# Performance work log

Hardware: AMD Instinct MI355X
Metric: run time of the kernel (lower is better)

Reference implementation:

```python
import math
import jax, jax.numpy as jnp
import numpy as np

HIDDEN = 2048
NUM_HEADS = 32
HEAD_DIM = HIDDEN // NUM_HEADS
NUM_BLOCKS = 4
INTER = 2 * HIDDEN
EPS = 1e-5
ROPE_THETA = 10000.0


def setup_inputs() -> dict:
    key = jax.random.key(0)
    ks = jax.random.split(key, 6)
    B, S = 2, 2048
    sc = 0.02
    return {
        "x": jax.random.normal(ks[0], (B, S, HIDDEN), jnp.float32),
        "attn_norm_w": jnp.ones((HIDDEN,), jnp.float32),
        "ffn_norm_w": jnp.ones((HIDDEN,), jnp.float32),
        "w_qkv": jax.random.normal(ks[1], (3 * HIDDEN, HIDDEN), jnp.float32) * sc,
        "w_o": jax.random.normal(ks[2], (HIDDEN, HIDDEN), jnp.float32) * sc,
        "w_up": jax.random.normal(ks[3], (2 * INTER, HIDDEN), jnp.float32) * sc,
        "w_down": jax.random.normal(ks[4], (HIDDEN, INTER), jnp.float32) * sc,
    }


def _rmsnorm(x, w):
    var = jnp.mean(x * x, axis=-1, keepdims=True)
    return x * jax.lax.rsqrt(var + EPS) * w


def _rope_cache(seq_len, dim, theta, scale):
    inv_freq = 1.0 / (theta ** (jnp.arange(0, dim, 2, dtype=jnp.float32) / dim))
    t = jnp.arange(seq_len, dtype=jnp.float32) / scale
    freqs = jnp.outer(t, inv_freq)                     # [S, D/2]
    emb = jnp.concatenate([freqs, freqs], axis=-1)     # [S, D]
    return jnp.cos(emb), jnp.sin(emb)


def _apply_rope(x, cos, sin):
    # x: [B, H, S, D]
    d2 = x.shape[-1] // 2
    x1, x2 = x[..., :d2], x[..., d2:]
    rot = jnp.concatenate([-x2, x1], axis=-1)
    return x * cos[None, None] + rot * sin[None, None]


def reference(x, attn_norm_w, ffn_norm_w, w_qkv, w_o, w_up, w_down):
    B, S, _ = x.shape
    residual = x
    h = _rmsnorm(x, attn_norm_w)

    qkv = jnp.einsum('bsh,oh->bso', h, w_qkv)
    qkv = qkv.reshape(B, S, 3, NUM_HEADS, HEAD_DIM)
    q, k, v = qkv[:, :, 0], qkv[:, :, 1], qkv[:, :, 2]
    q = q.transpose(0, 2, 1, 3)  # [B,H,S,D]
    k = k.transpose(0, 2, 1, 3)
    v = v.transpose(0, 2, 1, 3)

    cos, sin = _rope_cache(S, HEAD_DIM, ROPE_THETA, 1.0)
    q = _apply_rope(q, cos, sin)
    k = _apply_rope(k, cos, sin)

    scale = 1.0 / math.sqrt(HEAD_DIM)
    attn = jnp.einsum('bhqd,bhkd->bhqk', q, k) * scale

    num_blocks = max(1, min(NUM_BLOCKS, S))
    blk = math.ceil(S / num_blocks)
    pos = jnp.arange(S)
    block_ids = pos // blk
    block_mask = block_ids[:, None] != block_ids[None, :]
    causal_mask = pos[:, None] < pos[None, :]
    invalid = causal_mask | block_mask                 # [S,S]
    mask_floor = jnp.finfo(attn.dtype).min
    attn = jnp.where(invalid[None, None], mask_floor, attn)

    attn = jax.nn.softmax(attn, axis=-1)
    context = jnp.einsum('bhqk,bhkd->bhqd', attn, v)
    context = context.transpose(0, 2, 1, 3).reshape(B, S, HIDDEN)

    x = residual + jnp.einsum('bsh,oh->bso', context, w_o)

    residual = x
    h = _rmsnorm(x, ffn_norm_w)
    up = jnp.einsum('bsh,oh->bso', h, w_up)
    gate, value = up[..., :INTER], up[..., INTER:]
    down = jnp.einsum('bsi,oi->bso', jax.nn.silu(gate) * value, w_down)
    return residual + down
```

## Files before the change

kernel.cpp:

```cpp
#include <hip/hip_runtime.h>
#include <cstdint>
#include <cstddef>

typedef __bf16 bf16x8 __attribute__((ext_vector_type(8)));
typedef __bf16 bf16x4 __attribute__((ext_vector_type(4)));
typedef float  f32x4  __attribute__((ext_vector_type(4)));

#define TOKENS  4096
#define SEQLEN  2048
#define HID     2048
#define QKV_W   6144
#define UP_W    8192
#define INTER_  4096

__device__ __forceinline__ void async16(const void* g, void* l) {
  __builtin_amdgcn_global_load_lds(
      (__attribute__((address_space(1))) void*)(g),
      (__attribute__((address_space(3))) void*)(l), 16, 0, 0);
}

__global__ __launch_bounds__(256) void cvt_kernel(const float* __restrict__ src,
                                                  __bf16* __restrict__ dst, int n4) {
  int i = blockIdx.x * 256 + threadIdx.x;
  if (i >= n4) return;
  float4 f = ((const float4*)src)[i];
  bf16x4 o;
  o[0] = (__bf16)f.x; o[1] = (__bf16)f.y; o[2] = (__bf16)f.z; o[3] = (__bf16)f.w;
  ((bf16x4*)dst)[i] = o;
}

__global__ __launch_bounds__(256) void rmsnorm_kernel(const float* __restrict__ x,
                                                      const float* __restrict__ wgt,
                                                      __bf16* __restrict__ out) {
  const int tok = blockIdx.x;
  const int t = threadIdx.x;
  const float4* xr = (const float4*)(x + (long)tok * HID);
  float4 a = xr[t], b = xr[t + 256];
  float ss = a.x*a.x + a.y*a.y + a.z*a.z + a.w*a.w
           + b.x*b.x + b.y*b.y + b.z*b.z + b.w*b.w;
  #pragma unroll
  for (int off = 32; off; off >>= 1) ss += __shfl_xor(ss, off);
  __shared__ float red[4];
  if ((t & 63) == 0) red[t >> 6] = ss;
  __syncthreads();
  float tot = red[0] + red[1] + red[2] + red[3];
  float r = rsqrtf(tot * (1.0f / HID) + 1e-5f);
  const float4* wr = (const float4*)wgt;
  float4 wa = wr[t], wb = wr[t + 256];
  bf16x4 o0, o1;
  o0[0] = (__bf16)(a.x * r * wa.x); o0[1] = (__bf16)(a.y * r * wa.y);
  o0[2] = (__bf16)(a.z * r * wa.z); o0[3] = (__bf16)(a.w * r * wa.w);
  o1[0] = (__bf16)(b.x * r * wb.x); o1[1] = (__bf16)(b.y * r * wb.y);
  o1[2] = (__bf16)(b.z * r * wb.z); o1[3] = (__bf16)(b.w * r * wb.w);
  bf16x4* orow = (bf16x4*)(out + (long)tok * HID);
  orow[t] = o0; orow[t + 256] = o1;
}

template<bool OUT_BF16, bool ADD_RES, bool ROPE, bool SILU>
__global__ __launch_bounds__(256) void gemm_bt(const __bf16* __restrict__ A, int lda,
                                               const __bf16* __restrict__ B, int ldb,
                                               void* Cv, int ldc,
                                               const float* __restrict__ Res, int K) {
  __shared__ __align__(16) __bf16 As[128 * 64];
  __shared__ __align__(16) __bf16 Bs[128 * 64];
  const int t = threadIdx.x;
  const int lane = t & 63;
  const int w = t >> 6;
  const int wm = (w >> 1) * 64, wn = (w & 1) * 64;
  const int m0 = blockIdx.y * 128;
  const int n0 = SILU ? blockIdx.x * 64 : blockIdx.x * 128;
  const int sr = t >> 3;
  const int sc = (((t & 7) ^ (sr & 7)) * 8);
  const __bf16* Ag = A + (long)(m0 + sr) * lda + sc;
  const __bf16* Bg = B + (long)(n0 + sr) * ldb + sc;
  char* lA = (char*)As + t * 16;
  char* lB = (char*)Bs + t * 16;
  const int lr = lane & 15;
  const int lq = lane >> 4;
  f32x4 acc[4][4] = {};
  for (int k0 = 0; k0 < K; k0 += 64) {
    __syncthreads();
    #pragma unroll
    for (int c = 0; c < 4; c++)
      async16(Ag + (long)(c * 32) * lda + k0, lA + c * 4096);
    #pragma unroll
    for (int c = 0; c < 4; c++) {
      const long rowoff = SILU ? (long)((c & 1) * INTER_ + (c >> 1) * 32) * ldb
                               : (long)(c * 32) * ldb;
      async16(Bg + rowoff + k0, lB + c * 4096);
    }
    __syncthreads();
    #pragma unroll
    for (int ks = 0; ks < 2; ks++) {
      const int pos = (((ks * 4 + lq) ^ (lr & 7)) * 8);
      bf16x8 af[4], bfr[4];
      #pragma unroll
      for (int i = 0; i < 4; i++)
        af[i]  = *(const bf16x8*)(As + (wm + i * 16 + lr) * 64 + pos);
      #pragma unroll
      for (int j = 0; j < 4; j++)
        bfr[j] = *(const bf16x8*)(Bs + (wn + j * 16 + lr) * 64 + pos);
      #pragma unroll
      for (int i = 0; i < 4; i++)
        #pragma unroll
        for (int j = 0; j < 4; j++)
          acc[i][j] = __builtin_amdgcn_mfma_f32_16x16x32_bf16(af[i], bfr[j], acc[i][j], 0, 0, 0);
    }
  }
  const int lq4 = lq * 4;
  #pragma unroll
  for (int i = 0; i < 4; i++) {
    #pragma unroll
    for (int r = 0; r < 4; r++) {
      const long row = m0 + wm + i * 16 + lq4 + r;
      #pragma unroll
      for (int j = 0; j < 4; j++) {
        const long col = n0 + wn + j * 16 + lr;
        float v = acc[i][j][r];
        if (ADD_RES) v += Res[row * (long)ldc + col];
        if (OUT_BF16) ((__bf16*)Cv)[row * (long)ldc + col] = (__bf16)v;
        else          ((float*)Cv)[row * (long)ldc + col] = v;
      }
    }
  }
}

template<bool ROPE, bool SILU>
__global__ __launch_bounds__(512, 2) void gemm8p(const __bf16* __restrict__ A, int lda,
                                                 const __bf16* __restrict__ B, int ldb,
                                                 void* Cv, int ldc, int K) {
  __shared__ __align__(16) __bf16 As[2 * 16384];
  __shared__ __align__(16) __bf16 Bs[2 * 16384];
  const int tid  = threadIdx.x;
  const int lane = tid & 63;
  const int w    = tid >> 6;
  const int wm2  = w >> 2;
  const int wn4  = w & 3;
  const int lr   = lane & 15;
  const int lq   = lane >> 4;
  const int m0   = blockIdx.y * 256;
  const int n0   = ROPE ? blockIdx.x * 256 : 0;
  const int n0c  = SILU ? blockIdx.x * 128 : 0;

  const long r0 = tid >> 3;
  const int  e  = (((tid & 7) ^ ((int)r0 & 7)) * 8);
  const __bf16* Ap0 = A + (long)(m0 + r0) * lda + e;
  long br0, br1, bhs;
  if (ROPE) {
    br0 = n0 + 64 * (((int)r0 >> 5) & 3) + ((int)r0 & 31);
    br1 = n0 + 64 * ((((int)r0 + 64) >> 5) & 3) + ((int)r0 & 31);
    bhs = 32 * (long)ldb;
  } else {
    br0 = n0c + r0;
    br1 = n0c + r0 + 64;
    bhs = (long)INTER_ * ldb;
  }
  const __bf16* Bp0 = B + br0 * ldb + e;
  const __bf16* Bp1 = B + br1 * ldb + e;
  char* sA = (char*)As;
  char* sB = (char*)Bs;
  const int tid16 = tid * 16;

#define STAGE_A(h_, nb_, kk_) do {                                                     \
    async16(Ap0 + (long)((h_) * 128) * lda + (kk_),      sA + (nb_)*32768 + (h_)*16384 + tid16);        \
    async16(Ap0 + (long)((h_) * 128 + 64) * lda + (kk_), sA + (nb_)*32768 + (h_)*16384 + 8192 + tid16); \
  } while (0)
#define STAGE_B(h_, nb_, kk_) do {                                                     \
    async16(Bp0 + (h_) * bhs + (kk_), sB + (nb_)*32768 + (h_)*16384 + tid16);          \
    async16(Bp1 + (h_) * bhs + (kk_), sB + (nb_)*32768 + (h_)*16384 + 8192 + tid16);   \
  } while (0)

  const int ch0 = ((lq ^ (lr & 7)) * 16);
  const int ch1 = (((4 + lq) ^ (lr & 7)) * 16);
  const int abase = (wm2 * 64 + lr) * 128;
  const int bbase = (wn4 * 32 + lr) * 128;

  f32x4 acc[8][4] = {};
  bf16x8 af[4][2], bfr[4][2];
  const int NT = K >> 6;

#define LOAD_A(mh_) do {                                                               \
    _Pragma("unroll")                                                                  \
    for (int i = 0; i < 4; i++) {                                                      \
      af[i][0] = *(const bf16x8*)(Ab + abase + (mh_)*16384 + i*2048 + ch0);            \
      af[i][1] = *(const bf16x8*)(Ab + abase + (mh_)*16384 + i*2048 + ch1);            \
    } } while (0)
#define LOAD_B(nh_) do {                                                               \
    _Pragma("unroll")                                                                  \
    for (int j = 0; j < 2; j++) {                                                      \
      bfr[(nh_)*2 + j][0] = *(const bf16x8*)(Bb + bbase + (nh_)*16384 + j*2048 + ch0); \
      bfr[(nh_)*2 + j][1] = *(const bf16x8*)(Bb + bbase + (nh_)*16384 + j*2048 + ch1); \
    } } while (0)
#define MFMA_Q(mh_, nh_) do {                                                          \
    __builtin_amdgcn_s_setprio(1);                                                     \
    _Pragma("unroll")                                                                  \
    for (int ks = 0; ks < 2; ks++)                                                     \
      _Pragma("unroll")                                                                \
      for (int i = 0; i < 4; i++)                                                      \
        _Pragma("unroll")                                                              \
        for (int j = 0; j < 2; j++)                                                    \
          acc[(mh_)*4 + i][(nh_)*2 + j] = __builtin_amdgcn_mfma_f32_16x16x32_bf16(     \
              af[i][ks], bfr[(nh_)*2 + j][ks], acc[(mh_)*4 + i][(nh_)*2 + j], 0, 0, 0);\
    __builtin_amdgcn_s_setprio(0);                                                     \
  } while (0)
#define SBAR() do { __builtin_amdgcn_sched_barrier(0);                                 \
    __builtin_amdgcn_s_barrier(); __builtin_amdgcn_sched_barrier(0); } while (0)
#define LGKM0() do { asm volatile("s_waitcnt lgkmcnt(0)" ::: "memory");                \
    __builtin_amdgcn_sched_barrier(0); } while (0)

  STAGE_A(0, 0, 0); STAGE_B(0, 0, 0); STAGE_B(1, 0, 0); STAGE_A(1, 0, 0);
  asm volatile("s_waitcnt vmcnt(4)" ::: "memory");
  SBAR();

  for (int T = 0; T < NT; ++T) {
    const int cb = T & 1, nb = cb ^ 1;
    const int kk = (T + 1) << 6;
    const bool st = (T + 1 < NT);
    const char* Ab = (const char*)As + cb * 32768;
    const char* Bb = (const char*)Bs + cb * 32768;
    LOAD_A(0); LOAD_B(0);
    if (st) { STAGE_A(0, nb, kk); STAGE_B(0, nb, kk); }
    SBAR(); LGKM0();
    MFMA_Q(0, 0);
    if (st) asm volatile("s_waitcnt vmcnt(6)" ::: "memory");
    else    asm volatile("s_waitcnt vmcnt(2)" ::: "memory");
    SBAR();
    LOAD_B(1);
    if (st) STAGE_B(1, nb, kk);
    SBAR(); LGKM0();
    MFMA_Q(0, 1);
    if (st) asm volatile("s_waitcnt vmcnt(6)" ::: "memory");
    else    asm volatile("s_waitcnt vmcnt(0)" ::: "memory");
    SBAR();
    LOAD_A(1);
    if (st) STAGE_A(1, nb, kk);
    SBAR(); LGKM0();
    MFMA_Q(1, 0);
    SBAR();
    MFMA_Q(1, 1);
    if (st) asm volatile("s_waitcnt vmcnt(4)" ::: "memory");
    SBAR();
  }
#undef STAGE_A
#undef STAGE_B
#undef LOAD_A
#undef LOAD_B
#undef MFMA_Q
#undef SBAR
#undef LGKM0

  const int lq4 = lq * 4;
  if (ROPE) {
    if (n0 < 4096) {
      const float invf0 = exp2f((float)(lr)      * -0.41524101186092029f);
      const float invf1 = exp2f((float)(16 + lr) * -0.41524101186092029f);
      #pragma unroll
      for (int mi = 0; mi < 8; mi++) {
        #pragma unroll
        for (int r = 0; r < 4; r++) {
          const long row = m0 + (mi >> 2) * 128 + wm2 * 64 + (mi & 3) * 16 + lq4 + r;
          const float s = (float)(int)(row & (SEQLEN - 1));
          __bf16* crow = (__bf16*)Cv + row * (long)ldc + n0 + wn4 * 64 + lr;
          #pragma unroll
          for (int nj = 0; nj < 2; nj++) {
            float x1 = acc[mi][nj][r], x2 = acc[mi][nj + 2][r];
            float ang = s * (nj ? invf1 : invf0);
            float sn, cs;
            __sincosf(ang, &sn, &cs);
            crow[nj * 16]      = (__bf16)(x1 * cs - x2 * sn);
            crow[nj * 16 + 32] = (__bf16)(x2 * cs + x1 * sn);
          }
        }
      }
    } else {
      #pragma unroll
      for (int mi = 0; mi < 8; mi++) {
        #pragma unroll
        for (int r = 0; r < 4; r++) {
          const long row = m0 + (mi >> 2) * 128 + wm2 * 64 + (mi & 3) * 16 + lq4 + r;
          __bf16* crow = (__bf16*)Cv + row * (long)ldc + n0 + wn4 * 64 + lr;
          #pragma unroll
          for (int njf = 0; njf < 4; njf++)
            crow[(njf >> 1) * 32 + (njf & 1) * 16] = (__bf16)acc[mi][njf][r];
        }
      }
    }
  } else {
    #pragma unroll
    for (int mi = 0; mi < 8; mi++) {
      #pragma unroll
      for (int r = 0; r < 4; r++) {
        const long row = m0 + (mi >> 2) * 128 + wm2 * 64 + (mi & 3) * 16 + lq4 + r;
        #pragma unroll
        for (int nj = 0; nj < 2; nj++) {
          const long col = n0c + wn4 * 32 + nj * 16 + lr;
          float g = acc[mi][nj][r];
          float v = acc[mi][nj + 2][r];
          float sg = g / (1.0f + __expf(-g));
          ((__bf16*)Cv)[row * (long)ldc + col] = (__bf16)(sg * v);
        }
      }
    }
  }
}

__global__ __launch_bounds__(256) void attn_kernel(const __bf16* __restrict__ qkv,
                                                   __bf16* __restrict__ ctx) {
  const int qt   = blockIdx.x;
  const int head = blockIdx.y;
  const int b    = blockIdx.z;
  const int w    = threadIdx.x >> 6;
  const int lane = threadIdx.x & 63;
  const int lr = lane & 15;
  const int lq = lane >> 4;
  const int q0   = qt * 64;
  const int blk0 = q0 & ~511;
  const int nkv  = q0 + 64 - blk0;
  const int NT   = nkv >> 5;
  const long tok0 = (long)b * SEQLEN;

  const int qrow = q0 + w * 16 + lr;
  const long qoff = (tok0 + qrow) * QKV_W + head * 64 + lq * 8;
  bf16x8 qf0 = *(const bf16x8*)(qkv + qoff);
  bf16x8 qf1 = *(const bf16x8*)(qkv + qoff + 32);

  __shared__ __align__(16) char VTb[8192];
  __shared__ __align__(16) char Pbb[8192];

  const __bf16* kp = qkv + (tok0 + blk0 + lr) * QKV_W + HID + head * 64 + lq * 8;
  const int skv = threadIdx.x & 31;
  const int sd0 = (threadIdx.x >> 5) * 8;
  const __bf16* vp = qkv + (tok0 + blk0 + skv) * QKV_W + 2 * HID + head * 64 + sd0;

  bf16x8 ka[2][2], kb[2][2];

#define LOADK(KN, tk) do { \
    KN[0][0] = *(const bf16x8*)(kp + (long)(tk) * QKV_W); \
    KN[0][1] = *(const bf16x8*)(kp + (long)(tk) * QKV_W + 32); \
    KN[1][0] = *(const bf16x8*)(kp + (long)((tk) + 16) * QKV_W); \
    KN[1][1] = *(const bf16x8*)(kp + (long)((tk) + 16) * QKV_W + 32); \
  } while (0)

#define WRITEV(vr_, hb_) do { \
    const int c_ = (hb_) * 4 + (skv >> 3); \
    char* vb_ = VTb + sd0 * 128 + ((skv & 7) * 2); \
    _Pragma("unroll") \
    for (int i_ = 0; i_ < 8; i_++) \
      *(__bf16*)(vb_ + i_ * 128 + ((c_ ^ i_) * 16)) = vr_[i_]; \
  } while (0)

  LOADK(ka, 0);
  {
    bf16x8 vr0 = *(const bf16x8*)(vp);
    WRITEV(vr0, 0);
  }
  __syncthreads();

  float m[4], l[4];
  f32x4 oacc[4] = {};
  #pragma unroll
  for (int r = 0; r < 4; r++) { m[r] = -1e30f; l[r] = 0.0f; }
  const int myrow = q0 + w * 16 + lq * 4;

#define ITER(t_, hb_, KC, KN) { \
    const int tkn_ = ((t_) + 1) * 32; \
    const bool more_ = ((t_) + 1 < NT); \
    bf16x8 vr_ = {}; \
    if (more_) { LOADK(KN, tkn_); vr_ = *(const bf16x8*)(vp + (long)tkn_ * QKV_W); } \
    f32x4 s0 = {0.f, 0.f, 0.f, 0.f}, s1 = {0.f, 0.f, 0.f, 0.f}; \
    s0 = __builtin_amdgcn_mfma_f32_16x16x32_bf16(qf0, KC[0][0], s0, 0, 0, 0); \
    s0 = __builtin_amdgcn_mfma_f32_16x16x32_bf16(qf1, KC[0][1], s0, 0, 0, 0); \
    s1 = __builtin_amdgcn_mfma_f32_16x16x32_bf16(qf0, KC[1][0], s1, 0, 0, 0); \
    s1 = __builtin_amdgcn_mfma_f32_16x16x32_bf16(qf1, KC[1][1], s1, 0, 0, 0); \
    const int kpos0_ = blk0 + (t_) * 32 + lr; \
    float p0[4], p1[4], alpha[4]; \
    _Pragma("unroll") \
    for (int r = 0; r < 4; r++) { \
      float v0 = s0[r] * 0.125f, v1 = s1[r] * 0.125f; \
      v0 = (kpos0_      <= myrow + r) ? v0 : -1e30f; \
      v1 = (kpos0_ + 16 <= myrow + r) ? v1 : -1e30f; \
      float mx = fmaxf(v0, v1); \
      mx = fmaxf(mx, __shfl_xor(mx, 1)); \
      mx = fmaxf(mx, __shfl_xor(mx, 2)); \
      mx = fmaxf(mx, __shfl_xor(mx, 4)); \
      mx = fmaxf(mx, __shfl_xor(mx, 8)); \
      float mn = fmaxf(m[r], mx); \
      alpha[r] = __expf(m[r] - mn); \
      m[r] = mn; \
      p0[r] = __expf(v0 - mn); \
      p1[r] = __expf(v1 - mn); \
      float rs = p0[r] + p1[r]; \
      rs += __shfl_xor(rs, 1); rs += __shfl_xor(rs, 2); \
      rs += __shfl_xor(rs, 4); rs += __shfl_xor(rs, 8); \
      l[r] = l[r] * alpha[r] + rs; \
    } \
    _Pragma("unroll") \
    for (int dt = 0; dt < 4; dt++) \
      _Pragma("unroll") \
      for (int r = 0; r < 4; r++) oacc[dt][r] *= alpha[r]; \
    { \
      char* pw_ = Pbb + w * 2048 + (lq * 4) * 128 + ((lr & 7) * 2); \
      const int cl_ = (hb_) * 4 + (lr >> 3); \
      _Pragma("unroll") \
      for (int r = 0; r < 4; r++) { \
        const int q7_ = (lq * 4 + r) & 7; \
        *(__bf16*)(pw_ + r * 128 + (((cl_    ) ^ q7_) * 16)) = (__bf16)p0[r]; \
        *(__bf16*)(pw_ + r * 128 + (((cl_ + 2) ^ q7_) * 16)) = (__bf16)p1[r]; \
      } \
    } \
    asm volatile("s_waitcnt lgkmcnt(0)" ::: "memory"); \
    const int swz_ = (((hb_) * 4 + lq) ^ (lr & 7)) * 16; \
    bf16x8 pf_ = *(const bf16x8*)(Pbb + w * 2048 + lr * 128 + swz_); \
    _Pragma("unroll") \
    for (int dt = 0; dt < 4; dt++) { \
      bf16x8 vf_ = *(const bf16x8*)(VTb + dt * 2048 + lr * 128 + swz_); \
      oacc[dt] = __builtin_amdgcn_mfma_f32_16x16x32_bf16(pf_, vf_, oacc[dt], 0, 0, 0); \
    } \
    __syncthreads(); \
    if (more_) WRITEV(vr_, (hb_) ^ 1); \
    __syncthreads(); \
  }

  for (int t2 = 0; t2 < NT; t2 += 2) {
    ITER(t2, 0, ka, kb)
    ITER(t2 + 1, 1, kb, ka)
  }
#undef ITER
#undef LOADK
#undef WRITEV

  #pragma unroll
  for (int r = 0; r < 4; r++) {
    float inv = 1.0f / l[r];
    long obase = (tok0 + myrow + r) * HID + head * 64;
    #pragma unroll
    for (int dt = 0; dt < 4; dt++)
      ctx[obase + dt * 16 + lr] = (__bf16)(oacc[dt][r] * inv);
  }
}

extern "C" void kernel_launch(void* const* d_in, const int* in_sizes, int n_in,
                              void* d_out, int out_size, void* d_ws, size_t ws_size,
                              hipStream_t stream) {
  const float* x      = (const float*)d_in[0];
  const float* anw    = (const float*)d_in[1];
  const float* fnw    = (const float*)d_in[2];
  const float* w_qkv  = (const float*)d_in[3];
  const float* w_o    = (const float*)d_in[4];
  const float* w_up   = (const float*)d_in[5];
  const float* w_down = (const float*)d_in[6];
  float* out = (float*)d_out;

  char* wsb = (char*)d_ws;
  __bf16* ABUF = (__bf16*)wsb;
  __bf16* QKV  = (__bf16*)(wsb + (size_t)16777216);
  __bf16* WBUF = (__bf16*)(wsb + (size_t)83886080);
  __bf16* ACT  = QKV;

  rmsnorm_kernel<<<TOKENS, 256, 0, stream>>>(x, anw, ABUF);
  cvt_kernel<<<(QKV_W * HID / 4 + 255) / 256, 256, 0, stream>>>(w_qkv, WBUF, QKV_W * HID / 4);
  gemm8p<true, false><<<dim3(QKV_W / 256, TOKENS / 256), 512, 0, stream>>>(
      ABUF, HID, WBUF, HID, (void*)QKV, QKV_W, HID);
  attn_kernel<<<dim3(SEQLEN / 64, 32, 2), 256, 0, stream>>>(QKV, ABUF);
  cvt_kernel<<<(HID * HID / 4 + 255) / 256, 256, 0, stream>>>(w_o, WBUF, HID * HID / 4);
  gemm_bt<false, true, false, false><<<dim3(HID / 128, TOKENS / 128), 256, 0, stream>>>(
      ABUF, HID, WBUF, HID, (void*)out, HID, x, HID);

  rmsnorm_kernel<<<TOKENS, 256, 0, stream>>>(out, fnw, ABUF);
  cvt_kernel<<<(UP_W * HID / 4 + 255) / 256, 256, 0, stream>>>(w_up, WBUF, UP_W * HID / 4);
  gemm8p<false, true><<<dim3(INTER_ / 128, TOKENS / 256), 512, 0, stream>>>(
      ABUF, HID, WBUF, HID, (void*)ACT, INTER_, HID);
  cvt_kernel<<<(HID * INTER_ / 4 + 255) / 256, 256, 0, stream>>>(w_down, WBUF, HID * INTER_ / 4);
  gemm_bt<false, true, false, false><<<dim3(HID / 128, TOKENS / 128), 256, 0, stream>>>(
      ACT, INTER_, WBUF, INTER_, (void*)out, HID, out, INTER_);
}
```

Before: 566.2 us.

## Double-buffer LDS fragment registers to overlap shared reads with MFMA in GEMM

```diff
diff --git a/kernel.cpp b/kernel.cpp
--- a/kernel.cpp
+++ b/kernel.cpp
@@ -176,22 +176,24 @@
   const int bbase = (wn4 * 32 + lr) * 128;
 
   f32x4 acc[8][4] = {};
-  bf16x8 af[4][2], bfr[4][2];
+  bf16x8 afA[4][2], afB[4][2], b0f[2][2], b1f[2][2];
   const int NT = K >> 6;
 
-#define LOAD_A(mh_) do {                                                               \
+#define RD_A(dst_, half_, buf_) do {                                                   \
+    const char* p_ = (const char*)As + (buf_) * 32768 + (half_) * 16384 + abase;       \
     _Pragma("unroll")                                                                  \
     for (int i = 0; i < 4; i++) {                                                      \
-      af[i][0] = *(const bf16x8*)(Ab + abase + (mh_)*16384 + i*2048 + ch0);            \
-      af[i][1] = *(const bf16x8*)(Ab + abase + (mh_)*16384 + i*2048 + ch1);            \
+      dst_[i][0] = *(const bf16x8*)(p_ + i * 2048 + ch0);                              \
+      dst_[i][1] = *(const bf16x8*)(p_ + i * 2048 + ch1);                              \
     } } while (0)
-#define LOAD_B(nh_) do {                                                               \
+#define RD_B(dst_, half_, buf_) do {                                                   \
+    const char* p_ = (const char*)Bs + (buf_) * 32768 + (half_) * 16384 + bbase;       \
     _Pragma("unroll")                                                                  \
     for (int j = 0; j < 2; j++) {                                                      \
-      bfr[(nh_)*2 + j][0] = *(const bf16x8*)(Bb + bbase + (nh_)*16384 + j*2048 + ch0); \
-      bfr[(nh_)*2 + j][1] = *(const bf16x8*)(Bb + bbase + (nh_)*16384 + j*2048 + ch1); \
+      dst_[j][0] = *(const bf16x8*)(p_ + j * 2048 + ch0);                              \
+      dst_[j][1] = *(const bf16x8*)(p_ + j * 2048 + ch1);                              \
     } } while (0)
-#define MFMA_Q(mh_, nh_) do {                                                          \
+#define MFMA_Q2(mh_, Aset_, Bset_, nh_) do {                                           \
     __builtin_amdgcn_s_setprio(1);                                                     \
     _Pragma("unroll")                                                                  \
     for (int ks = 0; ks < 2; ks++)                                                     \
@@ -199,55 +201,58 @@
       for (int i = 0; i < 4; i++)                                                      \
         _Pragma("unroll")                                                              \
         for (int j = 0; j < 2; j++)                                                    \
-          acc[(mh_)*4 + i][(nh_)*2 + j] = __builtin_amdgcn_mfma_f32_16x16x32_bf16(     \
-              af[i][ks], bfr[(nh_)*2 + j][ks], acc[(mh_)*4 + i][(nh_)*2 + j], 0, 0, 0);\
+          acc[(mh_)*4+i][(nh_)*2+j] = __builtin_amdgcn_mfma_f32_16x16x32_bf16(         \
+              Aset_[i][ks], Bset_[j][ks], acc[(mh_)*4+i][(nh_)*2+j], 0, 0, 0);         \
     __builtin_amdgcn_s_setprio(0);                                                     \
   } while (0)
-#define SBAR() do { __builtin_amdgcn_sched_barrier(0);                                 \
-    __builtin_amdgcn_s_barrier(); __builtin_amdgcn_sched_barrier(0); } while (0)
-#define LGKM0() do { asm volatile("s_waitcnt lgkmcnt(0)" ::: "memory");                \
-    __builtin_amdgcn_sched_barrier(0); } while (0)
+#define BAR() __builtin_amdgcn_s_barrier()
+#define VMW(n_) asm volatile("s_waitcnt vmcnt(" #n_ ")" ::: "memory")
 
   STAGE_A(0, 0, 0); STAGE_B(0, 0, 0); STAGE_B(1, 0, 0); STAGE_A(1, 0, 0);
-  asm volatile("s_waitcnt vmcnt(4)" ::: "memory");
-  SBAR();
-
-  for (int T = 0; T < NT; ++T) {
+  VMW(2);
+  BAR();
+  RD_A(afA, 0, 0); RD_B(b0f, 0, 0);
+
+  for (int T = 0; T < NT - 1; ++T) {
     const int cb = T & 1, nb = cb ^ 1;
     const int kk = (T + 1) << 6;
-    const bool st = (T + 1 < NT);
-    const char* Ab = (const char*)As + cb * 32768;
-    const char* Bb = (const char*)Bs + cb * 32768;
-    LOAD_A(0); LOAD_B(0);
-    if (st) { STAGE_A(0, nb, kk); STAGE_B(0, nb, kk); }
-    SBAR(); LGKM0();
-    MFMA_Q(0, 0);
-    if (st) asm volatile("s_waitcnt vmcnt(6)" ::: "memory");
-    else    asm volatile("s_waitcnt vmcnt(2)" ::: "memory");
-    SBAR();
-    LOAD_B(1);
-    if (st) STAGE_B(1, nb, kk);
-    SBAR(); LGKM0();
-    MFMA_Q(0, 1);
-    if (st) asm volatile("s_waitcnt vmcnt(6)" ::: "memory");
-    else    asm volatile("s_waitcnt vmcnt(0)" ::: "memory");
-    SBAR();
-    LOAD_A(1);
-    if (st) STAGE_A(1, nb, kk);
-    SBAR(); LGKM0();
-    MFMA_Q(1, 0);
-    SBAR();
-    MFMA_Q(1, 1);
-    if (st) asm volatile("s_waitcnt vmcnt(4)" ::: "memory");
-    SBAR();
+    STAGE_A(0, nb, kk); STAGE_B(0, nb, kk);
+    RD_B(b1f, 1, cb);
+    MFMA_Q2(0, afA, b0f, 0);
+    VMW(4);
+    BAR();
+    STAGE_B(1, nb, kk);
+    RD_A(afB, 1, cb);
+    MFMA_Q2(0, afA, b1f, 1);
+    BAR();
+    STAGE_A(1, nb, kk);
+    MFMA_Q2(1, afB, b0f, 0);
+    VMW(4);
+    BAR();
+    RD_A(afA, 0, nb); RD_B(b0f, 0, nb);
+    MFMA_Q2(1, afB, b1f, 1);
+    VMW(2);
+    BAR();
+  }
+  {
+    const int cb = (NT - 1) & 1;
+    RD_B(b1f, 1, cb);
+    MFMA_Q2(0, afA, b0f, 0);
+    VMW(0);
+    BAR();
+    RD_A(afB, 1, cb);
+    MFMA_Q2(0, afA, b1f, 1);
+    BAR();
+    MFMA_Q2(1, afB, b0f, 0);
+    MFMA_Q2(1, afB, b1f, 1);
   }
 #undef STAGE_A
 #undef STAGE_B
-#undef LOAD_A
-#undef LOAD_B
-#undef MFMA_Q
-#undef SBAR
-#undef LGKM0
+#undef RD_A
+#undef RD_B
+#undef MFMA_Q2
+#undef BAR
+#undef VMW
 
   const int lq4 = lq * 4;
   if (ROPE) {
```

Measured after the change: 618.4 us, median of 2. 9.2% more time.
